# Kernel optimization log

Measured on AMD Instinct MI355X. Metric: run time of the kernel, lower is better.

Reference implementation:

```python
import jax, jax.numpy as jnp
import numpy as np
import math

PI = math.pi
N = 10000        # nodes
F_IN = 128       # num_features
NHID = 128       # nhid
NCLS = 16        # num_classes
HEADS = 2
E = 320000       # edges (avg degree 32)
GCN_IN = 7 * NHID  # (2^3 - 1) * nhid from 3-layer Haar scattering
NEG_SLOPE = 0.2  # GATConv leaky relu slope


def _phi(l):
    l = jnp.where(l == 0, 1e-7, l)
    y = 2 * PI * l
    return jnp.sin(y) / y


def _psi(l):
    l = jnp.where(l == 0, 1e-8, l)
    y = PI * l
    return jnp.sin(l) / y * (1 - jnp.cos(l))


def _prop3(x, lamb, V):
    # propLayerHaar, J=3: filters phi(8*lamb), psi(lamb/4), psi(lamb/2)
    Vt_x = V.T @ x                               # shared [N, F]
    hs = (_phi(8.0 * lamb), _psi(lamb / 4.0), _psi(lamb / 2.0))
    return [V @ (h[:, None] * Vt_x) for h in hs]


def _get_rep(x, lamb, V):
    # getRep with layer=3 -> 1 + 2 + 4 = 7 low-pass outputs, concat on features
    y = _prop3(x, lamb, V)
    out = [y[0]]
    nxt = y[1:]
    for _ in range(2):
        new_nxt = []
        for t in nxt:
            z = _prop3(jnp.abs(t), lamb, V)
            out.append(z[0])
            new_nxt += z[1:]
        nxt = new_nxt
    return jnp.concatenate(out, axis=1)         # [N, 7*F]


def _agg_add(x, src, dst):
    # MessagePassing(aggr='add') with message = x_j
    return jax.ops.segment_sum(x[src], dst, num_segments=N)


def _gat(x, src, dst, W, att_src, att_dst, bias):
    # PyG GATConv (concat heads, self-loops, eval mode -> no dropout)
    H, C = HEADS, NCLS
    h = (x @ W).reshape(N, H, C)                 # [N, H, C]
    a_src = jnp.einsum('nhc,hc->nh', h, att_src)
    a_dst = jnp.einsum('nhc,hc->nh', h, att_dst)
    loop = jnp.arange(N)
    s = jnp.concatenate([src, loop])
    d = jnp.concatenate([dst, loop])
    e = jax.nn.leaky_relu(a_src[s] + a_dst[d], NEG_SLOPE)   # [E+N, H]
    m = jax.ops.segment_max(e, d, num_segments=N)
    ex = jnp.exp(e - m[d])
    denom = jax.ops.segment_sum(ex, d, num_segments=N)
    alpha = ex / denom[d]                                   # softmax per dst
    out = jax.ops.segment_sum(alpha[:, :, None] * h[s], d, num_segments=N)
    return out.reshape(N, H * C) + bias


def setup_inputs() -> dict:
    key = jax.random.key(0)
    ks = jax.random.split(key, 12)
    x = jax.random.normal(ks[0], (N, F_IN), jnp.float32)
    edge_index = jax.random.randint(ks[1], (2, E), 0, N, dtype=jnp.int32).astype(jnp.int64)
    lamb = jax.random.uniform(ks[2], (N,), jnp.float32) * 2.0
    V = jax.random.normal(ks[3], (N, N), jnp.float32) / np.float32(np.sqrt(N))
    W1 = jax.random.normal(ks[4], (F_IN, NHID), jnp.float32) / np.float32(np.sqrt(F_IN))
    b1 = jnp.zeros((NHID,), jnp.float32)
    gat_W = jax.random.normal(ks[5], (GCN_IN, HEADS * NCLS), jnp.float32) / np.float32(np.sqrt(GCN_IN))
    att_src = jax.random.normal(ks[6], (HEADS, NCLS), jnp.float32) / np.float32(np.sqrt(NCLS))
    att_dst = jax.random.normal(ks[7], (HEADS, NCLS), jnp.float32) / np.float32(np.sqrt(NCLS))
    gat_bias = jnp.zeros((HEADS * NCLS,), jnp.float32)
    mlp_W = jax.random.normal(ks[8], (HEADS * NCLS, NCLS), jnp.float32) / np.float32(np.sqrt(HEADS * NCLS))
    mlp_b = jnp.zeros((NCLS,), jnp.float32)
    return {'x': x, 'edge_index': edge_index, 'lamb': lamb, 'V': V,
            'W1': W1, 'b1': b1, 'gat_W': gat_W, 'att_src': att_src,
            'att_dst': att_dst, 'gat_bias': gat_bias, 'mlp_W': mlp_W, 'mlp_b': mlp_b}


def reference(x, edge_index, lamb, V, W1, b1, gat_W, att_src, att_dst, gat_bias, mlp_W, mlp_b):
    src, dst = edge_index[0], edge_index[1]
    h = x @ W1 + b1                              # linear1: [N, nhid]
    rep = _get_rep(h, lamb, V)                   # [N, 7*nhid]
    agg = _agg_add(rep, src, dst)                # first propagate
    g = _gat(agg, src, dst, gat_W, att_src, att_dst, gat_bias)  # [N, 2*ncls]
    g = jax.nn.elu(g) @ mlp_W + mlp_b            # mlp (dropout = eval mode)
    out = _agg_add(g, src, dst)                  # second propagate
    return jax.nn.log_softmax(out, axis=1)
```

## Files before the change

kernel.cpp:

```cpp
#include <hip/hip_runtime.h>
#include <math.h>


#define NN     10000
#define KP     10048
#define NRPAD  10112
#define FIN    128
#define NHID   128
#define PIF    3.14159265358979323846f
#define LOSC   2048.0f
#define ILOSC  (1.0f/2048.0f)

typedef _Float16 f16x8 __attribute__((ext_vector_type(8)));
typedef _Float16 f16x4 __attribute__((ext_vector_type(4)));
typedef float    f32x4 __attribute__((ext_vector_type(4)));

__device__ __forceinline__ float lrelu(float x) { return x > 0.f ? x : 0.2f * x; }

__device__ __forceinline__ void split16(float v, _Float16* hi, _Float16* lo) {
    _Float16 h = (_Float16)v;
    *hi = h;
    *lo = (_Float16)((v - (float)h) * LOSC);
}

__device__ __forceinline__ void gload16(const void* g, void* l) {
    __builtin_amdgcn_global_load_lds((const __attribute__((address_space(1))) void*)g,
                                     (__attribute__((address_space(3))) void*)l, 16, 0, 0);
}

__global__ void k_filters(const float* __restrict__ lamb, float* __restrict__ filt) {
    int i = blockIdx.x * blockDim.x + threadIdx.x;
    if (i >= NN) return;
    float l = lamb[i];
    float a = 8.f * l; if (a == 0.f) a = 1e-7f;
    float ya = 2.f * PIF * a;
    filt[i] = sinf(ya) / ya;
    float b = l * 0.25f; if (b == 0.f) b = 1e-8f;
    filt[NN + i] = sinf(b) / (PIF * b) * (1.f - cosf(b));
    float c = l * 0.5f; if (c == 0.f) c = 1e-8f;
    filt[2 * NN + i] = sinf(c) / (PIF * c) * (1.f - cosf(c));
}

__global__ __launch_bounds__(256) void k_buildVT(const float* __restrict__ V,
                                                 _Float16* __restrict__ VTh,
                                                 _Float16* __restrict__ VTl) {
    __shared__ float t[32][33];
    int tx = threadIdx.x, ty = threadIdx.y;
    int k0 = blockIdx.x * 32, n0 = blockIdx.y * 32;
#pragma unroll
    for (int i = 0; i < 4; i++) {
        int k = k0 + ty * 4 + i, n = n0 + tx;
        t[ty * 4 + i][tx] = (k < NN && n < NN) ? V[(size_t)k * NN + n] : 0.f;
    }
    __syncthreads();
#pragma unroll
    for (int i = 0; i < 4; i++) {
        int n = n0 + ty * 4 + i, k = k0 + tx;
        if (n < NRPAD && k < KP) {
            _Float16 h, l; split16(t[tx][ty * 4 + i], &h, &l);
            VTh[(size_t)n * KP + k] = h;
            VTl[(size_t)n * KP + k] = l;
        }
    }
}

__global__ __launch_bounds__(256) void k_buildVr(const float* __restrict__ V,
                                                 _Float16* __restrict__ Vrh,
                                                 _Float16* __restrict__ Vrl) {
    int t = blockIdx.x * 256 + threadIdx.x;
    const int KQ = KP / 4;
    int n = t / KQ;
    if (n >= NRPAD) return;
    int k4 = (t - n * KQ) * 4;
    float4 v = make_float4(0.f, 0.f, 0.f, 0.f);
    if (n < NN && k4 < NN)
        v = *(const float4*)(V + (size_t)n * NN + k4);
    f16x4 h, l;
    _Float16 hh, ll;
    split16(v.x, &hh, &ll); h[0] = hh; l[0] = ll;
    split16(v.y, &hh, &ll); h[1] = hh; l[1] = ll;
    split16(v.z, &hh, &ll); h[2] = hh; l[2] = ll;
    split16(v.w, &hh, &ll); h[3] = hh; l[3] = ll;
    *(f16x4*)(Vrh + (size_t)n * KP + k4) = h;
    *(f16x4*)(Vrl + (size_t)n * KP + k4) = l;
}

__global__ __launch_bounds__(256) void k_xw1t(const float* __restrict__ x, const float* __restrict__ W1,
                                              const float* __restrict__ b1,
                                              _Float16* __restrict__ hTh, _Float16* __restrict__ hTl) {
    int n = blockIdx.x * 256 + threadIdx.x;
    int c = blockIdx.y;
    if (n >= KP) return;
    float acc = 0.f;
    if (n < NN) {
        acc = b1[c];
        const float* xr = x + (size_t)n * FIN;
#pragma unroll 4
        for (int k = 0; k < FIN; k++) acc += xr[k] * W1[k * NHID + c];
    }
    _Float16 h, l; split16(acc, &h, &l);
    hTh[(size_t)c * KP + n] = h;
    hTl[(size_t)c * KP + n] = l;
}

template<int MODE, int NF>
__global__ __launch_bounds__(256, 2) void k_mfma(
    const _Float16* __restrict__ Ah, const _Float16* __restrict__ Al,
    const _Float16* __restrict__ Bh, const _Float16* __restrict__ Bl,
    int C,
    const float* __restrict__ filt,
    _Float16* __restrict__ OutH, _Float16* __restrict__ OutL,
    float* __restrict__ Dy, int absStart,
    _Float16* __restrict__ XaH, _Float16* __restrict__ XaL)
{
    __shared__ __align__(16) _Float16 sAh[128 * 64];
    __shared__ __align__(16) _Float16 sAl[128 * 64];
    __shared__ __align__(16) _Float16 sBh[128 * 64];
    __shared__ __align__(16) _Float16 sBl[128 * 64];

    const int tid  = threadIdx.x;
    const int lane = tid & 63;
    const int wave = tid >> 6;
    const int arow0 = blockIdx.x * 128;
    const int brow0 = blockIdx.y * 128;

    const int lrow = lane >> 3;
    const int kcol = ((lane & 7) ^ lrow) << 3;
    size_t offA[4], offB[4];
#pragma unroll
    for (int r = 0; r < 4; ++r) {
        int rit = wave * 32 + r * 8 + lrow;
        offA[r] = (size_t)(arow0 + rit) * KP + kcol;
        offB[r] = (size_t)(brow0 + rit) * KP + kcol;
    }

    f32x4 acc1[4][4], acc2[4][4];
#pragma unroll
    for (int i = 0; i < 4; ++i)
#pragma unroll
        for (int j = 0; j < 4; ++j) { acc1[i][j] = 0.f; acc2[i][j] = 0.f; }

    const int fr = lane & 15;
    const int fg = lane >> 4;
    const int wr = (wave >> 1) * 64;
    const int wc = (wave & 1) * 64;

    for (int kt = 0; kt < KP / 64; ++kt) {
        const size_t ko = (size_t)kt * 64;
#pragma unroll
        for (int r = 0; r < 4; ++r) {
            int cc = (wave * 4 + r) * 512;
            gload16(Ah + offA[r] + ko, sAh + cc);
            gload16(Al + offA[r] + ko, sAl + cc);
            gload16(Bh + offB[r] + ko, sBh + cc);
            gload16(Bl + offB[r] + ko, sBl + cc);
        }
        __syncthreads();
#pragma unroll
        for (int ki = 0; ki < 2; ++ki) {
            const int cs = ((((ki << 2) | fg)) ^ (fr & 7)) << 3;
            f16x8 ah[4], al[4], bh[4], bl[4];
#pragma unroll
            for (int mt = 0; mt < 4; ++mt) {
                int off = (wr + mt * 16 + fr) * 64 + cs;
                ah[mt] = *(const f16x8*)(sAh + off);
                al[mt] = *(const f16x8*)(sAl + off);
            }
#pragma unroll
            for (int nt = 0; nt < 4; ++nt) {
                int off = (wc + nt * 16 + fr) * 64 + cs;
                bh[nt] = *(const f16x8*)(sBh + off);
                bl[nt] = *(const f16x8*)(sBl + off);
            }
#pragma unroll
            for (int mt = 0; mt < 4; ++mt)
#pragma unroll
                for (int nt = 0; nt < 4; ++nt) {
                    acc1[mt][nt] = __builtin_amdgcn_mfma_f32_16x16x32_f16(ah[mt], bh[nt], acc1[mt][nt], 0, 0, 0);
                    acc2[mt][nt] = __builtin_amdgcn_mfma_f32_16x16x32_f16(ah[mt], bl[nt], acc2[mt][nt], 0, 0, 0);
                    acc2[mt][nt] = __builtin_amdgcn_mfma_f32_16x16x32_f16(al[mt], bh[nt], acc2[mt][nt], 0, 0, 0);
                }
        }
        __syncthreads();
    }

    const int ccol  = lane & 15;
    const int crow0 = (lane >> 4) * 4;
#pragma unroll
    for (int nt = 0; nt < 4; ++nt) {
        int n = brow0 + wc + nt * 16 + ccol;
        if (n >= KP) continue;
        bool valid = n < NN;
        float f0 = 0.f, f1 = 0.f, f2 = 0.f;
        if (MODE == 0 && valid) {
            f0 = filt[n];
            if (NF > 1) { f1 = filt[NN + n]; f2 = filt[2 * NN + n]; }
        }
#pragma unroll
        for (int mt = 0; mt < 4; ++mt) {
            int cb = arow0 + wr + mt * 16 + crow0;
#pragma unroll
            for (int r = 0; r < 4; ++r) {
                float v = acc1[mt][nt][r] + acc2[mt][nt][r] * ILOSC;
                int c = cb + r;
                if (MODE == 0) {
#pragma unroll
                    for (int f = 0; f < NF; ++f) {
                        float fv = (f == 0 ? f0 : (f == 1 ? f1 : f2)) * v;
                        _Float16 h, l; split16(fv, &h, &l);
                        size_t o = (size_t)(f * C + c) * KP + n;
                        OutH[o] = h; OutL[o] = l;
                    }
                } else {
                    if (valid) Dy[(size_t)c * NN + n] = v;
                    if (c >= absStart) {
                        float av = valid ? fabsf(v) : 0.f;
                        _Float16 h, l; split16(av, &h, &l);
                        size_t o = (size_t)(c - absStart) * KP + n;
                        XaH[o] = h; XaL[o] = l;
                    }
                }
            }
        }
    }
}

__global__ void k_y2h2(const float* __restrict__ Yt, int c0, int C,
                       const float* __restrict__ Wp, float* __restrict__ r2) {
    int t = blockIdx.x * blockDim.x + threadIdx.x;
    if (t >= NN * 32) return;
    int n = t >> 5, j = t & 31;
    float acc = 0.f;
    for (int k = 0; k < C; k++) acc += Yt[(size_t)(c0 + k) * NN + n] * Wp[k * 32 + j];
    r2[t] += acc;
}

__global__ void k_zero_f(float* p, int n) {
    int i = blockIdx.x * blockDim.x + threadIdx.x;
    if (i < n) p[i] = 0.f;
}

__global__ void k_zero_int(int* p, int n) {
    int i = blockIdx.x * blockDim.x + threadIdx.x;
    if (i < n) p[i] = 0;
}
__global__ void k_count(const int* __restrict__ dst, int* __restrict__ deg, int E) {
    int e = blockIdx.x * blockDim.x + threadIdx.x;
    if (e < E) atomicAdd(&deg[dst[e]], 1);
}
__global__ __launch_bounds__(1024) void k_scan(const int* __restrict__ deg,
                                               int* __restrict__ rowp, int* __restrict__ cur, int E) {
    __shared__ int s[1024];
    int t = threadIdx.x;
    int base = t * 10;
    int sum = 0;
    for (int i = 0; i < 10; i++) { int idx = base + i; if (idx < NN) sum += deg[idx]; }
    s[t] = sum; __syncthreads();
    for (int off = 1; off < 1024; off <<= 1) {
        int v = (t >= off) ? s[t - off] : 0;
        __syncthreads();
        s[t] += v;
        __syncthreads();
    }
    int run = (t > 0) ? s[t - 1] : 0;
    for (int i = 0; i < 10; i++) {
        int idx = base + i;
        if (idx < NN) { rowp[idx] = run; cur[idx] = run; run += deg[idx]; }
    }
    if (t == 0) rowp[NN] = E;
}
__global__ void k_fill(const int* __restrict__ src, const int* __restrict__ dst,
                       int* __restrict__ cur, int* __restrict__ csr, int E) {
    int e = blockIdx.x * blockDim.x + threadIdx.x;
    if (e < E) {
        int d = dst[e];
        int p = atomicAdd(&cur[d], 1);
        csr[p] = src[e];
    }
}

__global__ void k_agg32(const float* __restrict__ r2, const int* __restrict__ rowp,
                        const int* __restrict__ csr, float* __restrict__ h2) {
    int t = blockIdx.x * blockDim.x + threadIdx.x;
    if (t >= NN * 32) return;
    int n = t >> 5, j = t & 31;
    int s0 = rowp[n], s1 = rowp[n + 1];
    float a = 0.f;
    for (int e = s0; e < s1; e++) a += r2[(size_t)csr[e] * 32 + j];
    h2[t] = a;
}

__global__ void k_att(const float* __restrict__ h2, const float* __restrict__ att_s,
                      const float* __restrict__ att_d, float* __restrict__ asrc,
                      float* __restrict__ adst) {
    int t = blockIdx.x * blockDim.x + threadIdx.x;
    if (t >= NN * 2) return;
    int n = t >> 1, hh = t & 1;
    const float* hr = h2 + (size_t)n * 32 + hh * 16;
    float s = 0.f, d = 0.f;
    for (int c = 0; c < 16; c++) {
        float v = hr[c];
        s += v * att_s[hh * 16 + c];
        d += v * att_d[hh * 16 + c];
    }
    asrc[t] = s; adst[t] = d;
}

__global__ __launch_bounds__(64) void k_gat(const float* __restrict__ h2,
                                            const float* __restrict__ asrc,
                                            const float* __restrict__ adst,
                                            const int* __restrict__ rowp,
                                            const int* __restrict__ csr,
                                            const float* __restrict__ bias,
                                            float* __restrict__ gout) {
    int d = blockIdx.x, lane = threadIdx.x;
    int s0 = rowp[d], s1 = rowp[d + 1];
    __shared__ float sm[2], sden[2];
    int hh = lane >> 5;
    float adh = adst[d * 2 + hh];
    float eself = lrelu(asrc[d * 2 + hh] + adh);
    float m = eself;
    for (int j = s0 + (lane & 31); j < s1; j += 32) {
        int s = csr[j];
        m = fmaxf(m, lrelu(asrc[s * 2 + hh] + adh));
    }
    for (int off = 16; off; off >>= 1) m = fmaxf(m, __shfl_xor(m, off, 32));
    float den = ((lane & 31) == 0) ? expf(eself - m) : 0.f;
    for (int j = s0 + (lane & 31); j < s1; j += 32) {
        int s = csr[j];
        den += expf(lrelu(asrc[s * 2 + hh] + adh) - m);
    }
    for (int off = 16; off; off >>= 1) den += __shfl_xor(den, off, 32);
    if ((lane & 31) == 0) { sm[hh] = m; sden[hh] = den; }
    __syncthreads();
    int f = lane & 31;
    int h3 = f >> 4;
    float mh = sm[h3], dh = sden[h3];
    float ad3 = adst[d * 2 + h3];
    float acc = 0.f;
    for (int j = s0 + (lane >> 5); j < s1; j += 2) {
        int s = csr[j];
        float e = lrelu(asrc[s * 2 + h3] + ad3);
        acc += expf(e - mh) * h2[(size_t)s * 32 + f];
    }
    if ((lane >> 5) == 0) {
        float es = lrelu(asrc[d * 2 + h3] + ad3);
        acc += expf(es - mh) * h2[(size_t)d * 32 + f];
    }
    acc += __shfl_down(acc, 32, 64);
    if (lane < 32) gout[(size_t)d * 32 + f] = acc / dh + bias[f];
}

__global__ void k_mlp(const float* __restrict__ gout, const float* __restrict__ mw,
                      const float* __restrict__ mb, float* __restrict__ g) {
    int t = blockIdx.x * blockDim.x + threadIdx.x;
    if (t >= NN * 16) return;
    int n = t >> 4, j = t & 15;
    const float* gr = gout + (size_t)n * 32;
    float acc = mb[j];
    for (int k = 0; k < 32; k++) {
        float v = gr[k];
        v = v > 0.f ? v : expm1f(v);
        acc += v * mw[k * 16 + j];
    }
    g[t] = acc;
}

__global__ __launch_bounds__(64) void k_final(const float* __restrict__ g,
                                              const int* __restrict__ rowp,
                                              const int* __restrict__ csr,
                                              float* __restrict__ out) {
    int d = blockIdx.x, lane = threadIdx.x;
    int s0 = rowp[d], s1 = rowp[d + 1];
    int f = lane & 15, grp = lane >> 4;
    float acc = 0.f;
    for (int j = s0 + grp; j < s1; j += 4) acc += g[(size_t)csr[j] * 16 + f];
    acc += __shfl_xor(acc, 16, 64);
    acc += __shfl_xor(acc, 32, 64);
    float mx = acc;
    for (int off = 8; off; off >>= 1) mx = fmaxf(mx, __shfl_xor(mx, off, 16));
    float ex = expf(acc - mx);
    float se = ex;
    for (int off = 8; off; off >>= 1) se += __shfl_xor(se, off, 16);
    if (lane < 16) out[(size_t)d * 16 + f] = acc - mx - logf(se);
}

extern "C" void kernel_launch(void* const* d_in, const int* in_sizes, int n_in,
                              void* d_out, int out_size, void* d_ws, size_t ws_size,
                              hipStream_t stream) {
    (void)n_in; (void)out_size; (void)ws_size;
    const float* x       = (const float*)d_in[0];
    const int*   ei      = (const int*)d_in[1];
    const float* lamb    = (const float*)d_in[2];
    const float* V       = (const float*)d_in[3];
    const float* W1      = (const float*)d_in[4];
    const float* b1      = (const float*)d_in[5];
    const float* gat_W   = (const float*)d_in[6];
    const float* att_src = (const float*)d_in[7];
    const float* att_dst = (const float*)d_in[8];
    const float* gat_b   = (const float*)d_in[9];
    const float* mlp_W   = (const float*)d_in[10];
    const float* mlp_b   = (const float*)d_in[11];
    float* out = (float*)d_out;
    const int E = in_sizes[1] / 2;
    const int* e_src = ei;
    const int* e_dst = ei + E;

    char* w = (char*)d_ws;
    auto alloc = [&](size_t bytes) { void* p = (void*)w; w += (bytes + 255) & ~(size_t)255; return p; };
    _Float16* VTh  = (_Float16*)alloc((size_t)NRPAD * KP * 2);
    _Float16* VTl  = (_Float16*)alloc((size_t)NRPAD * KP * 2);
    _Float16* Vrh  = (_Float16*)alloc((size_t)NRPAD * KP * 2);
    _Float16* Vrl  = (_Float16*)alloc((size_t)NRPAD * KP * 2);
    _Float16* hTh  = (_Float16*)alloc((size_t)128 * KP * 2);
    _Float16* hTl  = (_Float16*)alloc((size_t)128 * KP * 2);
    _Float16* Bb0h = (_Float16*)alloc((size_t)384 * KP * 2);
    _Float16* Bb0l = (_Float16*)alloc((size_t)384 * KP * 2);
    _Float16* Xa1h = (_Float16*)alloc((size_t)256 * KP * 2);
    _Float16* Xa1l = (_Float16*)alloc((size_t)256 * KP * 2);
    _Float16* Bb1h = (_Float16*)alloc((size_t)768 * KP * 2);
    _Float16* Bb1l = (_Float16*)alloc((size_t)768 * KP * 2);
    _Float16* Xa2h = (_Float16*)alloc((size_t)512 * KP * 2);
    _Float16* Xa2l = (_Float16*)alloc((size_t)512 * KP * 2);
    _Float16* Bb2h = (_Float16*)alloc((size_t)512 * KP * 2);
    _Float16* Bb2l = (_Float16*)alloc((size_t)512 * KP * 2);
    float* Dy   = (float*)alloc((size_t)768 * NN * 4);
    float* r2   = (float*)alloc((size_t)NN * 32 * 4);
    float* h2   = (float*)alloc((size_t)NN * 32 * 4);
    float* asrc = (float*)alloc((size_t)NN * 2 * 4);
    float* adst = (float*)alloc((size_t)NN * 2 * 4);
    float* gout = (float*)alloc((size_t)NN * 32 * 4);
    float* g    = (float*)alloc((size_t)NN * 16 * 4);
    float* filt = (float*)alloc((size_t)3 * NN * 4);
    int* deg    = (int*)alloc((size_t)NN * 4);
    int* rowp   = (int*)alloc((size_t)(NN + 1) * 4);
    int* cur    = (int*)alloc((size_t)NN * 4);
    int* csr    = (int*)alloc((size_t)E * 4);

    k_zero_int<<<(NN + 255) / 256, 256, 0, stream>>>(deg, NN);
    k_count<<<(E + 255) / 256, 256, 0, stream>>>(e_dst, deg, E);
    k_scan<<<1, 1024, 0, stream>>>(deg, rowp, cur, E);
    k_fill<<<(E + 255) / 256, 256, 0, stream>>>(e_src, e_dst, cur, csr, E);

    k_filters<<<(NN + 255) / 256, 256, 0, stream>>>(lamb, filt);
    k_buildVT<<<dim3(KP / 32, NRPAD / 32), dim3(32, 8), 0, stream>>>(V, VTh, VTl);
    {
        long long tot = (long long)NRPAD * (KP / 4);
        k_buildVr<<<(int)((tot + 255) / 256), 256, 0, stream>>>(V, Vrh, Vrl);
    }
    k_xw1t<<<dim3((KP + 255) / 256, NHID), 256, 0, stream>>>(x, W1, b1, hTh, hTl);
    k_zero_f<<<(NN * 32 + 255) / 256, 256, 0, stream>>>(r2, NN * 32);

    const int NT = NRPAD / 128;

    k_mfma<0, 3><<<dim3(128 / 128, NT), 256, 0, stream>>>(hTh, hTl, VTh, VTl, 128, filt,
                                                          Bb0h, Bb0l, nullptr, 0, nullptr, nullptr);
    k_mfma<1, 0><<<dim3(384 / 128, NT), 256, 0, stream>>>(Bb0h, Bb0l, Vrh, Vrl, 384, nullptr,
                                                          nullptr, nullptr, Dy, 128, Xa1h, Xa1l);
    k_y2h2<<<(NN * 32 + 255) / 256, 256, 0, stream>>>(Dy, 0, 128, gat_W + 0 * 32, r2);

    k_mfma<0, 3><<<dim3(256 / 128, NT), 256, 0, stream>>>(Xa1h, Xa1l, VTh, VTl, 256, filt,
                                                          Bb1h, Bb1l, nullptr, 0, nullptr, nullptr);
    k_mfma<1, 0><<<dim3(768 / 128, NT), 256, 0, stream>>>(Bb1h, Bb1l, Vrh, Vrl, 768, nullptr,
                                                          nullptr, nullptr, Dy, 256, Xa2h, Xa2l);
    k_y2h2<<<(NN * 32 + 255) / 256, 256, 0, stream>>>(Dy, 0, 256, gat_W + 128 * 32, r2);

    k_mfma<0, 1><<<dim3(512 / 128, NT), 256, 0, stream>>>(Xa2h, Xa2l, VTh, VTl, 512, filt,
                                                          Bb2h, Bb2l, nullptr, 0, nullptr, nullptr);
    k_mfma<1, 0><<<dim3(512 / 128, NT), 256, 0, stream>>>(Bb2h, Bb2l, Vrh, Vrl, 512, nullptr,
                                                          nullptr, nullptr, Dy, 512, nullptr, nullptr);
    k_y2h2<<<(NN * 32 + 255) / 256, 256, 0, stream>>>(Dy, 0,   128, gat_W + 384 * 32, r2);
    k_y2h2<<<(NN * 32 + 255) / 256, 256, 0, stream>>>(Dy, 128, 128, gat_W + 640 * 32, r2);
    k_y2h2<<<(NN * 32 + 255) / 256, 256, 0, stream>>>(Dy, 256, 128, gat_W + 512 * 32, r2);
    k_y2h2<<<(NN * 32 + 255) / 256, 256, 0, stream>>>(Dy, 384, 128, gat_W + 768 * 32, r2);

    k_agg32<<<(NN * 32 + 255) / 256, 256, 0, stream>>>(r2, rowp, csr, h2);
    k_att<<<(NN * 2 + 255) / 256, 256, 0, stream>>>(h2, att_src, att_dst, asrc, adst);
    k_gat<<<NN, 64, 0, stream>>>(h2, asrc, adst, rowp, csr, gat_b, gout);
    k_mlp<<<(NN * 16 + 255) / 256, 256, 0, stream>>>(gout, mlp_W, mlp_b, g);
    k_final<<<NN, 64, 0, stream>>>(g, rowp, csr, out);
}
```

Baseline: 3.795 ms.

## Use smaller A-tiles with XCD-aware block remap and fuse V conversion kernels

The MFMA GEMM kernel gains a template tile height (32/64/128 rows of A), so the skinny GEMMs launch many more workgroups on a 1-D grid. Block ids are remapped so neighbouring tiles sharing B rows land on the same XCD, which should improve L2 reuse. The two V fp16-split kernels are fused into one pass that reads V once, and the x@W1 projection is split into a coalesced GEMV plus a transposing split kernel. Smaller tiles raise occupancy and parallelism but lower the MFMA work per byte loaded.

After: 3.346 ms. 11.8% less time.

```diff
diff --git a/kernel.cpp b/kernel.cpp
--- a/kernel.cpp
+++ b/kernel.cpp
@@ -41,141 +41,172 @@
     filt[2 * NN + i] = sinf(c) / (PIF * c) * (1.f - cosf(c));
 }
 
-__global__ __launch_bounds__(256) void k_buildVT(const float* __restrict__ V,
-                                                 _Float16* __restrict__ VTh,
-                                                 _Float16* __restrict__ VTl) {
-    __shared__ float t[32][33];
-    int tx = threadIdx.x, ty = threadIdx.y;
-    int k0 = blockIdx.x * 32, n0 = blockIdx.y * 32;
-#pragma unroll
-    for (int i = 0; i < 4; i++) {
-        int k = k0 + ty * 4 + i, n = n0 + tx;
-        t[ty * 4 + i][tx] = (k < NN && n < NN) ? V[(size_t)k * NN + n] : 0.f;
+__global__ __launch_bounds__(256) void k_buildV(const float* __restrict__ V,
+                                                _Float16* __restrict__ VTh,
+                                                _Float16* __restrict__ VTl,
+                                                _Float16* __restrict__ Vrh,
+                                                _Float16* __restrict__ Vrl) {
+    __shared__ float ts[32][33];
+    int t = threadIdx.x;
+    int row = t >> 3, c4 = (t & 7) * 4;
+    int j0 = blockIdx.x * 32;
+    int i0 = blockIdx.y * 32;
+    int i = i0 + row;
+    float4 v = make_float4(0.f, 0.f, 0.f, 0.f);
+    if (i < NN && j0 + c4 < NN)
+        v = *(const float4*)(V + (size_t)i * NN + j0 + c4);
+    ts[row][c4 + 0] = v.x; ts[row][c4 + 1] = v.y;
+    ts[row][c4 + 2] = v.z; ts[row][c4 + 3] = v.w;
+    if (j0 + c4 < KP) {
+        f16x4 h, l; _Float16 hh, ll;
+        split16(v.x, &hh, &ll); h[0] = hh; l[0] = ll;
+        split16(v.y, &hh, &ll); h[1] = hh; l[1] = ll;
+        split16(v.z, &hh, &ll); h[2] = hh; l[2] = ll;
+        split16(v.w, &hh, &ll); h[3] = hh; l[3] = ll;
+        *(f16x4*)(Vrh + (size_t)i * KP + j0 + c4) = h;
+        *(f16x4*)(Vrl + (size_t)i * KP + j0 + c4) = l;
     }
     __syncthreads();
-#pragma unroll
-    for (int i = 0; i < 4; i++) {
-        int n = n0 + ty * 4 + i, k = k0 + tx;
-        if (n < NRPAD && k < KP) {
-            _Float16 h, l; split16(t[tx][ty * 4 + i], &h, &l);
-            VTh[(size_t)n * KP + k] = h;
-            VTl[(size_t)n * KP + k] = l;
-        }
-    }
-}
-
-__global__ __launch_bounds__(256) void k_buildVr(const float* __restrict__ V,
-                                                 _Float16* __restrict__ Vrh,
-                                                 _Float16* __restrict__ Vrl) {
-    int t = blockIdx.x * 256 + threadIdx.x;
-    const int KQ = KP / 4;
-    int n = t / KQ;
-    if (n >= NRPAD) return;
-    int k4 = (t - n * KQ) * 4;
+    if (i0 + c4 < KP) {
+        f16x4 h, l; _Float16 hh, ll;
+        split16(ts[c4 + 0][row], &hh, &ll); h[0] = hh; l[0] = ll;
+        split16(ts[c4 + 1][row], &hh, &ll); h[1] = hh; l[1] = ll;
+        split16(ts[c4 + 2][row], &hh, &ll); h[2] = hh; l[2] = ll;
+        split16(ts[c4 + 3][row], &hh, &ll); h[3] = hh; l[3] = ll;
+        *(f16x4*)(VTh + (size_t)(j0 + row) * KP + i0 + c4) = h;
+        *(f16x4*)(VTl + (size_t)(j0 + row) * KP + i0 + c4) = l;
+    }
+}
+
+__global__ void k_xw1(const float* __restrict__ x, const float* __restrict__ W1,
+                      const float* __restrict__ b1, float* __restrict__ h) {
+    int t = blockIdx.x * blockDim.x + threadIdx.x;
+    if (t >= NN * NHID) return;
+    int n = t >> 7, j = t & 127;
+    const float* xr = x + (size_t)n * FIN;
+    float acc = b1[j];
+#pragma unroll 4
+    for (int k = 0; k < FIN; k++) acc += xr[k] * W1[k * NHID + j];
+    h[t] = acc;
+}
+
+__global__ __launch_bounds__(256) void k_hsplit(const float* __restrict__ h,
+                                                _Float16* __restrict__ hTh,
+                                                _Float16* __restrict__ hTl) {
+    __shared__ float ts[32][33];
+    int t = threadIdx.x;
+    int row = t >> 3, c4 = (t & 7) * 4;
+    int n0 = blockIdx.x * 32;
+    int c0 = blockIdx.y * 32;
+    int n = n0 + row;
     float4 v = make_float4(0.f, 0.f, 0.f, 0.f);
-    if (n < NN && k4 < NN)
-        v = *(const float4*)(V + (size_t)n * NN + k4);
-    f16x4 h, l;
-    _Float16 hh, ll;
-    split16(v.x, &hh, &ll); h[0] = hh; l[0] = ll;
-    split16(v.y, &hh, &ll); h[1] = hh; l[1] = ll;
-    split16(v.z, &hh, &ll); h[2] = hh; l[2] = ll;
-    split16(v.w, &hh, &ll); h[3] = hh; l[3] = ll;
-    *(f16x4*)(Vrh + (size_t)n * KP + k4) = h;
-    *(f16x4*)(Vrl + (size_t)n * KP + k4) = l;
-}
-
-__global__ __launch_bounds__(256) void k_xw1t(const float* __restrict__ x, const float* __restrict__ W1,
-                                              const float* __restrict__ b1,
-                                              _Float16* __restrict__ hTh, _Float16* __restrict__ hTl) {
-    int n = blockIdx.x * 256 + threadIdx.x;
-    int c = blockIdx.y;
-    if (n >= KP) return;
-    float acc = 0.f;
-    if (n < NN) {
-        acc = b1[c];
-        const float* xr = x + (size_t)n * FIN;
-#pragma unroll 4
-        for (int k = 0; k < FIN; k++) acc += xr[k] * W1[k * NHID + c];
-    }
-    _Float16 h, l; split16(acc, &h, &l);
-    hTh[(size_t)c * KP + n] = h;
-    hTl[(size_t)c * KP + n] = l;
-}
-
-template<int MODE, int NF>
+    if (n < NN)
+        v = *(const float4*)(h + (size_t)n * NHID + c0 + c4);
+    ts[row][c4 + 0] = v.x; ts[row][c4 + 1] = v.y;
+    ts[row][c4 + 2] = v.z; ts[row][c4 + 3] = v.w;
+    __syncthreads();
+    f16x4 hh4, ll4; _Float16 hh, ll;
+    split16(ts[c4 + 0][row], &hh, &ll); hh4[0] = hh; ll4[0] = ll;
+    split16(ts[c4 + 1][row], &hh, &ll); hh4[1] = hh; ll4[1] = ll;
+    split16(ts[c4 + 2][row], &hh, &ll); hh4[2] = hh; ll4[2] = ll;
+    split16(ts[c4 + 3][row], &hh, &ll); hh4[3] = hh; ll4[3] = ll;
+    *(f16x4*)(hTh + (size_t)(c0 + row) * KP + n0 + c4) = hh4;
+    *(f16x4*)(hTl + (size_t)(c0 + row) * KP + n0 + c4) = ll4;
+}
+
+template<int MODE, int NF, int TM>
 __global__ __launch_bounds__(256, 2) void k_mfma(
     const _Float16* __restrict__ Ah, const _Float16* __restrict__ Al,
     const _Float16* __restrict__ Bh, const _Float16* __restrict__ Bl,
-    int C,
+    int C, int MT,
     const float* __restrict__ filt,
     _Float16* __restrict__ OutH, _Float16* __restrict__ OutL,
     float* __restrict__ Dy, int absStart,
     _Float16* __restrict__ XaH, _Float16* __restrict__ XaL)
 {
-    __shared__ __align__(16) _Float16 sAh[128 * 64];
-    __shared__ __align__(16) _Float16 sAl[128 * 64];
+    constexpr int AM   = (TM == 32) ? 2 : 4;
+    constexpr int BN   = (TM == 128) ? 4 : 2;
+    constexpr int TU_A = TM / 8;
+    constexpr int TU   = (TM + 128) / 8;
+    constexpr int UPW  = TU / 4;
+
+    __shared__ __align__(16) _Float16 sAh[TM * 64];
+    __shared__ __align__(16) _Float16 sAl[TM * 64];
     __shared__ __align__(16) _Float16 sBh[128 * 64];
     __shared__ __align__(16) _Float16 sBl[128 * 64];
 
     const int tid  = threadIdx.x;
     const int lane = tid & 63;
     const int wave = tid >> 6;
-    const int arow0 = blockIdx.x * 128;
-    const int brow0 = blockIdx.y * 128;
+
+    const int nwg = (int)gridDim.x;
+    const int bid = (int)blockIdx.x;
+    const int q = nwg >> 3, r = nwg & 7;
+    const int xcd = bid & 7, lid = bid >> 3;
+    const int wg = (xcd < r ? xcd * (q + 1) : r * (q + 1) + (xcd - r) * q) + lid;
+    const int arow0 = (wg % MT) * TM;
+    const int brow0 = (wg / MT) * 128;
 
     const int lrow = lane >> 3;
     const int kcol = ((lane & 7) ^ lrow) << 3;
-    size_t offA[4], offB[4];
-#pragma unroll
-    for (int r = 0; r < 4; ++r) {
-        int rit = wave * 32 + r * 8 + lrow;
-        offA[r] = (size_t)(arow0 + rit) * KP + kcol;
-        offB[r] = (size_t)(brow0 + rit) * KP + kcol;
-    }
-
-    f32x4 acc1[4][4], acc2[4][4];
-#pragma unroll
-    for (int i = 0; i < 4; ++i)
-#pragma unroll
-        for (int j = 0; j < 4; ++j) { acc1[i][j] = 0.f; acc2[i][j] = 0.f; }
+    size_t offU[UPW]; int ldsU[UPW]; bool aU[UPW];
+#pragma unroll
+    for (int u = 0; u < UPW; ++u) {
+        int g = wave * UPW + u;
+        if (g < TU_A) {
+            aU[u] = true;  ldsU[u] = g * 512;
+            offU[u] = (size_t)(arow0 + g * 8 + lrow) * KP + kcol;
+        } else {
+            int b = g - TU_A;
+            aU[u] = false; ldsU[u] = b * 512;
+            offU[u] = (size_t)(brow0 + b * 8 + lrow) * KP + kcol;
+        }
+    }
+
+    f32x4 acc1[AM][BN], acc2[AM][BN];
+#pragma unroll
+    for (int i = 0; i < AM; ++i)
+#pragma unroll
+        for (int j = 0; j < BN; ++j) { acc1[i][j] = 0.f; acc2[i][j] = 0.f; }
 
     const int fr = lane & 15;
     const int fg = lane >> 4;
-    const int wr = (wave >> 1) * 64;
-    const int wc = (wave & 1) * 64;
+    const int wr = (TM == 128) ? (wave >> 1) * 64 : 0;
+    const int wc = (TM == 128) ? (wave & 1) * 64 : wave * 32;
 
     for (int kt = 0; kt < KP / 64; ++kt) {
         const size_t ko = (size_t)kt * 64;
 #pragma unroll
-        for (int r = 0; r < 4; ++r) {
-            int cc = (wave * 4 + r) * 512;
-            gload16(Ah + offA[r] + ko, sAh + cc);
-            gload16(Al + offA[r] + ko, sAl + cc);
-            gload16(Bh + offB[r] + ko, sBh + cc);
-            gload16(Bl + offB[r] + ko, sBl + cc);
+        for (int u = 0; u < UPW; ++u) {
+            if (aU[u]) {
+                gload16(Ah + offU[u] + ko, sAh + ldsU[u]);
+                gload16(Al + offU[u] + ko, sAl + ldsU[u]);
+            } else {
+                gload16(Bh + offU[u] + ko, sBh + ldsU[u]);
+                gload16(Bl + offU[u] + ko, sBl + ldsU[u]);
+            }
         }
         __syncthreads();
 #pragma unroll
         for (int ki = 0; ki < 2; ++ki) {
             const int cs = ((((ki << 2) | fg)) ^ (fr & 7)) << 3;
-            f16x8 ah[4], al[4], bh[4], bl[4];
-#pragma unroll
-            for (int mt = 0; mt < 4; ++mt) {
+            f16x8 ah[AM], al[AM], bh[BN], bl[BN];
+#pragma unroll
+            for (int mt = 0; mt < AM; ++mt) {
                 int off = (wr + mt * 16 + fr) * 64 + cs;
                 ah[mt] = *(const f16x8*)(sAh + off);
                 al[mt] = *(const f16x8*)(sAl + off);
             }
 #pragma unroll
-            for (int nt = 0; nt < 4; ++nt) {
+            for (int nt = 0; nt < BN; ++nt) {
                 int off = (wc + nt * 16 + fr) * 64 + cs;
                 bh[nt] = *(const f16x8*)(sBh + off);
                 bl[nt] = *(const f16x8*)(sBl + off);
             }
 #pragma unroll
-            for (int mt = 0; mt < 4; ++mt)
-#pragma unroll
-                for (int nt = 0; nt < 4; ++nt) {
+            for (int mt = 0; mt < AM; ++mt)
+#pragma unroll
+                for (int nt = 0; nt < BN; ++nt) {
                     acc1[mt][nt] = __builtin_amdgcn_mfma_f32_16x16x32_f16(ah[mt], bh[nt], acc1[mt][nt], 0, 0, 0);
                     acc2[mt][nt] = __builtin_amdgcn_mfma_f32_16x16x32_f16(ah[mt], bl[nt], acc2[mt][nt], 0, 0, 0);
                     acc2[mt][nt] = __builtin_amdgcn_mfma_f32_16x16x32_f16(al[mt], bh[nt], acc2[mt][nt], 0, 0, 0);
@@ -187,7 +218,7 @@
     const int ccol  = lane & 15;
     const int crow0 = (lane >> 4) * 4;
 #pragma unroll
-    for (int nt = 0; nt < 4; ++nt) {
+    for (int nt = 0; nt < BN; ++nt) {
         int n = brow0 + wc + nt * 16 + ccol;
         if (n >= KP) continue;
         bool valid = n < NN;
@@ -197,12 +228,12 @@
             if (NF > 1) { f1 = filt[NN + n]; f2 = filt[2 * NN + n]; }
         }
 #pragma unroll
-        for (int mt = 0; mt < 4; ++mt) {
+        for (int mt = 0; mt < AM; ++mt) {
             int cb = arow0 + wr + mt * 16 + crow0;
 #pragma unroll
-            for (int r = 0; r < 4; ++r) {
-                float v = acc1[mt][nt][r] + acc2[mt][nt][r] * ILOSC;
-                int c = cb + r;
+            for (int r2 = 0; r2 < 4; ++r2) {
+                float v = acc1[mt][nt][r2] + acc2[mt][nt][r2] * ILOSC;
+                int c = cb + r2;
                 if (MODE == 0) {
 #pragma unroll
                     for (int f = 0; f < NF; ++f) {
@@ -425,6 +456,7 @@
     _Float16* Bb2h = (_Float16*)alloc((size_t)512 * KP * 2);
     _Float16* Bb2l = (_Float16*)alloc((size_t)512 * KP * 2);
     float* Dy   = (float*)alloc((size_t)768 * NN * 4);
+    float* h    = (float*)alloc((size_t)NN * NHID * 4);
     float* r2   = (float*)alloc((size_t)NN * 32 * 4);
     float* h2   = (float*)alloc((size_t)NN * 32 * 4);
     float* asrc = (float*)alloc((size_t)NN * 2 * 4);
@@ -443,32 +475,29 @@
     k_fill<<<(E + 255) / 256, 256, 0, stream>>>(e_src, e_dst, cur, csr, E);
 
     k_filters<<<(NN + 255) / 256, 256, 0, stream>>>(lamb, filt);
-    k_buildVT<<<dim3(KP / 32, NRPAD / 32), dim3(32, 8), 0, stream>>>(V, VTh, VTl);
-    {
-        long long tot = (long long)NRPAD * (KP / 4);
-        k_buildVr<<<(int)((tot + 255) / 256), 256, 0, stream>>>(V, Vrh, Vrl);
-    }
-    k_xw1t<<<dim3((KP + 255) / 256, NHID), 256, 0, stream>>>(x, W1, b1, hTh, hTl);
+    k_buildV<<<dim3(NRPAD / 32, NRPAD / 32), 256, 0, stream>>>(V, VTh, VTl, Vrh, Vrl);
+    k_xw1<<<(NN * NHID + 255) / 256, 256, 0, stream>>>(x, W1, b1, h);
+    k_hsplit<<<dim3(KP / 32, NHID / 32), 256, 0, stream>>>(h, hTh, hTl);
     k_zero_f<<<(NN * 32 + 255) / 256, 256, 0, stream>>>(r2, NN * 32);
 
     const int NT = NRPAD / 128;
 
-    k_mfma<0, 3><<<dim3(128 / 128, NT), 256, 0, stream>>>(hTh, hTl, VTh, VTl, 128, filt,
-                                                          Bb0h, Bb0l, nullptr, 0, nullptr, nullptr);
-    k_mfma<1, 0><<<dim3(384 / 128, NT), 256, 0, stream>>>(Bb0h, Bb0l, Vrh, Vrl, 384, nullptr,
-                                                          nullptr, nullptr, Dy, 128, Xa1h, Xa1l);
+    k_mfma<0, 3, 32><<<4 * NT, 256, 0, stream>>>(hTh, hTl, VTh, VTl, 128, 4, filt,
+                                                 Bb0h, Bb0l, nullptr, 0, nullptr, nullptr);
+    k_mfma<1, 0, 64><<<6 * NT, 256, 0, stream>>>(Bb0h, Bb0l, Vrh, Vrl, 384, 6, nullptr,
+                                                 nullptr, nullptr, Dy, 128, Xa1h, Xa1l);
     k_y2h2<<<(NN * 32 + 255) / 256, 256, 0, stream>>>(Dy, 0, 128, gat_W + 0 * 32, r2);
 
-    k_mfma<0, 3><<<dim3(256 / 128, NT), 256, 0, stream>>>(Xa1h, Xa1l, VTh, VTl, 256, filt,
-                                                          Bb1h, Bb1l, nullptr, 0, nullptr, nullptr);
-    k_mfma<1, 0><<<dim3(768 / 128, NT), 256, 0, stream>>>(Bb1h, Bb1l, Vrh, Vrl, 768, nullptr,
-                                                          nullptr, nullptr, Dy, 256, Xa2h, Xa2l);
+    k_mfma<0, 3, 32><<<8 * NT, 256, 0, stream>>>(Xa1h, Xa1l, VTh, VTl, 256, 8, filt,
+                                                 Bb1h, Bb1l, nullptr, 0, nullptr, nullptr);
+    k_mfma<1, 0, 128><<<6 * NT, 256, 0, stream>>>(Bb1h, Bb1l, Vrh, Vrl, 768, 6, nullptr,
+                                                  nullptr, nullptr, Dy, 256, Xa2h, Xa2l);
     k_y2h2<<<(NN * 32 + 255) / 256, 256, 0, stream>>>(Dy, 0, 256, gat_W + 128 * 32, r2);
 
-    k_mfma<0, 1><<<dim3(512 / 128, NT), 256, 0, stream>>>(Xa2h, Xa2l, VTh, VTl, 512, filt,
-                                                          Bb2h, Bb2l, nullptr, 0, nullptr, nullptr);
-    k_mfma<1, 0><<<dim3(512 / 128, NT), 256, 0, stream>>>(Bb2h, Bb2l, Vrh, Vrl, 512, nullptr,
-                                                          nullptr, nullptr, Dy, 512, nullptr, nullptr);
+    k_mfma<0, 1, 64><<<8 * NT, 256, 0, stream>>>(Xa2h, Xa2l, VTh, VTl, 512, 8, filt,
+                                                 Bb2h, Bb2l, nullptr, 0, nullptr, nullptr);
+    k_mfma<1, 0, 64><<<8 * NT, 256, 0, stream>>>(Bb2h, Bb2l, Vrh, Vrl, 512, 8, nullptr,
+                                                 nullptr, nullptr, Dy, 512, nullptr, nullptr);
     k_y2h2<<<(NN * 32 + 255) / 256, 256, 0, stream>>>(Dy, 0,   128, gat_W + 384 * 32, r2);
     k_y2h2<<<(NN * 32 + 255) / 256, 256, 0, stream>>>(Dy, 128, 128, gat_W + 640 * 32, r2);
     k_y2h2<<<(NN * 32 + 255) / 256, 256, 0, stream>>>(Dy, 256, 128, gat_W + 512 * 32, r2);
```
